# Kernel optimization log

Measured on AMD Instinct MI355X. Metric: run time of the kernel, lower is better.

## Reference

```python
import jax, jax.numpy as jnp
import numpy as np

N, E, G = 150000, 300000, 4096   # nodes, edges, graphs
H, L = 256, 7                    # hidden_channels, num_gc_layers
ATOM_FEATS, ATOM_VOCAB = 9, 64
BOND_FEATS, BOND_VOCAB = 3, 8
BN_EPS = 1e-5
MSG_EPS = 1e-7


def setup_inputs() -> dict:
    key = jax.random.key(0)
    ks = jax.random.split(key, 10)
    return dict(
        x=jax.random.randint(ks[0], (N, ATOM_FEATS), 0, ATOM_VOCAB),
        edge_index=jax.random.randint(ks[1], (2, E), 0, N),
        edge_attr=jax.random.randint(ks[2], (E, BOND_FEATS), 0, BOND_VOCAB),
        batch=jnp.sort(jax.random.randint(ks[3], (N,), 0, G)),
        atom_emb=jax.random.normal(ks[4], (ATOM_FEATS, ATOM_VOCAB, H), jnp.float32) * 0.02,
        bond_emb=jax.random.normal(ks[5], (BOND_FEATS, BOND_VOCAB, H), jnp.float32) * 0.02,
        vn_weight=jnp.zeros((1, H), jnp.float32),  # Embedding(1,H) init to 0
        conv_w=jax.random.normal(ks[6], (L, H, H), jnp.float32) / np.float32(np.sqrt(H)),
        conv_b=jnp.zeros((L, H), jnp.float32),
        norm_gamma=jnp.ones((L, H), jnp.float32),
        norm_beta=jnp.zeros((L, H), jnp.float32),
        vn_w=jax.random.normal(ks[7], (L - 1, 2, H, H), jnp.float32) / np.float32(np.sqrt(H)),
        vn_b=jnp.zeros((L - 1, 2, H), jnp.float32),
        vn_gamma=jnp.ones((L - 1, 2, H), jnp.float32),
        vn_beta=jnp.zeros((L - 1, 2, H), jnp.float32),
    )


def _bn(x, gamma, beta):
    # BatchNorm1d in training mode (biased batch stats over the node axis)
    mu = jnp.mean(x, axis=0)
    var = jnp.mean(jnp.square(x - mu), axis=0)
    return (x - mu) * jax.lax.rsqrt(var + BN_EPS) * gamma + beta


def _genconv(h, src, dst, edge_emb, w, b):
    # GENConv, aggr='add', mlp_layers=1: msg = relu(x_j + e) + eps; out = Linear(x + sum_agg)
    msg = jax.nn.relu(h[src] + edge_emb) + MSG_EPS            # [E,H]
    agg = jax.ops.segment_sum(msg, dst, num_segments=N)       # [N,H]
    return (h + agg) @ w + b


def reference(x, edge_index, edge_attr, batch, atom_emb, bond_emb, vn_weight,
              conv_w, conv_b, norm_gamma, norm_beta, vn_w, vn_b, vn_gamma, vn_beta):
    src, dst = edge_index[0], edge_index[1]
    # AtomEncoder: sum of per-feature embeddings
    h = jnp.take(atom_emb[0], x[:, 0], axis=0)
    for f in range(1, ATOM_FEATS):
        h = h + jnp.take(atom_emb[f], x[:, f], axis=0)
    # virtual node embedding (one per graph, gathered init from Embedding(1,H))
    vn = jnp.broadcast_to(vn_weight[0], (G, H))
    h = h + vn[batch]
    # BondEncoder (conv_encode_edge=False -> encode once)
    edge_emb = jnp.take(bond_emb[0], edge_attr[:, 0], axis=0)
    for f in range(1, BOND_FEATS):
        edge_emb = edge_emb + jnp.take(bond_emb[f], edge_attr[:, f], axis=0)
    # res+ block: GENConv -> [BN -> ReLU -> VN update -> GENConv -> +res]*
    h = _genconv(h, src, dst, edge_emb, conv_w[0], conv_b[0])
    for layer in range(1, L):
        h2 = jax.nn.relu(_bn(h, norm_gamma[layer - 1], norm_beta[layer - 1]))
        # virtual node: pool + residual, 2-layer MLP (Linear->BN->ReLU twice)
        vn_t = jax.ops.segment_sum(h2, batch, num_segments=G) + vn
        for j in range(2):
            vn_t = jax.nn.relu(_bn(vn_t @ vn_w[layer - 1, j] + vn_b[layer - 1, j],
                                   vn_gamma[layer - 1, j], vn_beta[layer - 1, j]))
        vn = vn_t
        h2 = h2 + vn[batch]
        h = _genconv(h2, src, dst, edge_emb, conv_w[layer], conv_b[layer]) + h
    h = _bn(h, norm_gamma[L - 1], norm_beta[L - 1])
    return jax.ops.segment_sum(h, batch, num_segments=G)  # global_add_pool -> [G,H]
```

## Files before the change

kernel.cpp:

```cpp
#include <hip/hip_runtime.h>
#include <hip/hip_bf16.h>


#define Ncnt 150000
#define Ecnt 300000
#define Gcnt 4096
#define Hc 256
#define Lcnt 7
#define BN_EPS 1e-5f
#define MSG_EPS 1e-7f

typedef __hip_bfloat16 bf16;
typedef __attribute__((ext_vector_type(8))) short bf16x8;
typedef __attribute__((ext_vector_type(8))) unsigned short u16x8;
typedef __attribute__((ext_vector_type(4))) float f32x4;

static __device__ __forceinline__ int imin(int a, int b) { return a < b ? a : b; }

static __device__ __forceinline__ float bs2f(unsigned short s) {
  unsigned u = ((unsigned)s) << 16;
  union { unsigned u; float f; } c; c.u = u; return c.f;
}
static __device__ __forceinline__ unsigned short f2bs(float f) {
  bf16 h = __float2bfloat16(f);
  union { bf16 h; unsigned short s; } c; c.h = h; return c.s;
}
static __device__ __forceinline__ float4 bf4tof4(ushort4 u) {
  float4 r; r.x = bs2f(u.x); r.y = bs2f(u.y); r.z = bs2f(u.z); r.w = bs2f(u.w); return r;
}
static __device__ __forceinline__ ushort4 f4tobf4(float4 v) {
  ushort4 u; u.x = f2bs(v.x); u.y = f2bs(v.y); u.z = f2bs(v.z); u.w = f2bs(v.w); return u;
}

static __device__ __forceinline__ void gll16(const bf16* g, const short* l) {
  __builtin_amdgcn_global_load_lds((const __attribute__((address_space(1))) void*)g,
                                   (__attribute__((address_space(3))) void*)l, 16, 0, 0);
}

__global__ __launch_bounds__(256) void k_zero(float* __restrict__ p, int n) {
  int i = blockIdx.x * 256 + threadIdx.x;
  if (i < n) p[i] = 0.f;
}
__global__ __launch_bounds__(256) void k_zero_int(int* __restrict__ p, int n) {
  int i = blockIdx.x * 256 + threadIdx.x;
  if (i < n) p[i] = 0;
}
__global__ __launch_bounds__(256) void k_copy4(float* __restrict__ dst, const float* __restrict__ src, int n4) {
  int i = blockIdx.x * 256 + threadIdx.x;
  if (i < n4) ((float4*)dst)[i] = ((const float4*)src)[i];
}
__global__ void k_diag(float* __restrict__ out, float v) { out[0] = v; }

__global__ __launch_bounds__(256) void k_count(const int* __restrict__ ei, int* __restrict__ cnt) {
  int e = blockIdx.x * 256 + threadIdx.x;
  if (e < Ecnt) atomicAdd(&cnt[ei[Ecnt + e]], 1);
}
__global__ __launch_bounds__(256) void k_scan1(const int* __restrict__ cnt, int* __restrict__ rowptr,
                                               int* __restrict__ bsum, int n) {
  __shared__ int sh[256];
  int t = threadIdx.x;
  int i = blockIdx.x * 256 + t;
  int v = (i < n) ? cnt[i] : 0;
  sh[t] = v;
  __syncthreads();
#pragma unroll
  for (int off = 1; off < 256; off <<= 1) {
    int u = (t >= off) ? sh[t - off] : 0;
    __syncthreads();
    sh[t] += u;
    __syncthreads();
  }
  if (i < n) rowptr[i] = sh[t] - v;
  if (t == 255) bsum[blockIdx.x] = sh[255];
}
__global__ __launch_bounds__(1024) void k_scan2(int* __restrict__ bsum, int nb) {
  __shared__ int sh[1024];
  int t = threadIdx.x;
  int v = (t < nb) ? bsum[t] : 0;
  sh[t] = v;
  __syncthreads();
#pragma unroll
  for (int off = 1; off < 1024; off <<= 1) {
    int u = (t >= off) ? sh[t - off] : 0;
    __syncthreads();
    sh[t] += u;
    __syncthreads();
  }
  if (t < nb) bsum[t] = sh[t] - v;
}
__global__ __launch_bounds__(256) void k_scan3(int* __restrict__ rowptr, int* __restrict__ cursor,
                                               const int* __restrict__ bsum, int n) {
  int i = blockIdx.x * 256 + threadIdx.x;
  if (i < n) {
    int v = rowptr[i] + bsum[blockIdx.x];
    rowptr[i] = v;
    cursor[i] = v;
  }
  if (i == 0) rowptr[n] = Ecnt;
}
__global__ __launch_bounds__(256) void k_scatter(const int* __restrict__ ei, int* __restrict__ cursor,
                                                 int* __restrict__ eidx) {
  int e = blockIdx.x * 256 + threadIdx.x;
  if (e < Ecnt) {
    int d = ei[Ecnt + e];
    int pos = atomicAdd(&cursor[d], 1);
    eidx[pos] = e;
  }
}

__global__ __launch_bounds__(256) void k_prep_w(const float* __restrict__ W, bf16* __restrict__ hi,
                                                bf16* __restrict__ lo, int nmats) {
  int c = blockIdx.x * 256 + threadIdx.x;
  if (c >= nmats * 8192) return;
  int lane = c & 63;
  int t = c >> 6;
  int kc8 = t & 7;
  int nt = (t >> 3) & 15;
  int m = t >> 7;
  int n = nt * 16 + (lane & 15);
  int k0 = kc8 * 32 + (lane >> 4) * 8;
  bf16x8 hv, lv;
#pragma unroll
  for (int j = 0; j < 8; ++j) {
    float w = W[(size_t)m * 65536 + (size_t)(k0 + j) * 256 + n];
    unsigned short h = f2bs(w);
    float res = w - bs2f(h);
    hv[j] = (short)h;
    lv[j] = (short)f2bs(res);
  }
  *(bf16x8*)&hi[(size_t)c * 8] = hv;
  *(bf16x8*)&lo[(size_t)c * 8] = lv;
}

__global__ __launch_bounds__(256) void k_atom_encode(const int* __restrict__ x,
                                                     const float* __restrict__ aemb,
                                                     const float* __restrict__ vnw,
                                                     bf16* __restrict__ P) {
  int wave = threadIdx.x >> 6, lane = threadIdx.x & 63;
  int r = blockIdx.x * 4 + wave;
  if (r >= Ncnt) return;
  int c4 = lane * 4;
  const int* xr = x + (size_t)r * 9;
  float4 v = *(const float4*)&vnw[c4];
#pragma unroll
  for (int f = 0; f < 9; ++f) {
    float4 e = *(const float4*)&aemb[(size_t)((f << 6) + xr[f]) * Hc + c4];
    v.x += e.x; v.y += e.y; v.z += e.z; v.w += e.w;
  }
  *(ushort4*)&P[(size_t)r * Hc + c4] = f4tobf4(v);
}

__global__ __launch_bounds__(256) void k_init_vn(float* __restrict__ vn, const float* __restrict__ vnw) {
  int idx = blockIdx.x * 256 + threadIdx.x;
  vn[idx] = vnw[idx & (Hc - 1)];
}

__global__ __launch_bounds__(256) void k_agg(const bf16* __restrict__ P, bf16* __restrict__ T,
                                             const int* __restrict__ rowptr, const int* __restrict__ eidx,
                                             const int* __restrict__ ei, const int* __restrict__ ea,
                                             const float* __restrict__ bemb,
                                             const float* __restrict__ vn, const int* __restrict__ batch,
                                             const float* __restrict__ stats,
                                             const float* __restrict__ gamma, const float* __restrict__ beta,
                                             float invM) {
  int wave = threadIdx.x >> 6, lane = threadIdx.x & 63;
  int r = blockIdx.x * 4 + wave;
  if (r >= Ncnt) return;
  int c4 = lane * 4;
  bool hasbn = (stats != nullptr);
  float4 scv = make_float4(1.f, 1.f, 1.f, 1.f), bbv = make_float4(0.f, 0.f, 0.f, 0.f);
  if (hasbn) {
    float4 sv = *(const float4*)&stats[c4];
    float4 qv = *(const float4*)&stats[Hc + c4];
    float4 gv = *(const float4*)&gamma[c4];
    float4 bv = *(const float4*)&beta[c4];
    float mu, var;
    mu = sv.x * invM; var = qv.x * invM - mu * mu; scv.x = rsqrtf(var + BN_EPS) * gv.x; bbv.x = bv.x - mu * scv.x;
    mu = sv.y * invM; var = qv.y * invM - mu * mu; scv.y = rsqrtf(var + BN_EPS) * gv.y; bbv.y = bv.y - mu * scv.y;
    mu = sv.z * invM; var = qv.z * invM - mu * mu; scv.z = rsqrtf(var + BN_EPS) * gv.z; bbv.z = bv.z - mu * scv.z;
    mu = sv.w * invM; var = qv.w * invM - mu * mu; scv.w = rsqrtf(var + BN_EPS) * gv.w; bbv.w = bv.w - mu * scv.w;
  }
  float4 acc;
  {
    float4 v = bf4tof4(*(const ushort4*)&P[(size_t)r * Hc + c4]);
    if (hasbn) {
      v.x = fmaxf(fmaf(v.x, scv.x, bbv.x), 0.f); v.y = fmaxf(fmaf(v.y, scv.y, bbv.y), 0.f);
      v.z = fmaxf(fmaf(v.z, scv.z, bbv.z), 0.f); v.w = fmaxf(fmaf(v.w, scv.w, bbv.w), 0.f);
      const float4 w = *(const float4*)&vn[(size_t)batch[r] * Hc + c4];
      v.x += w.x; v.y += w.y; v.z += w.z; v.w += w.w;
    }
    acc = v;
  }
  int j1 = rowptr[r + 1];
  for (int j = rowptr[r]; j < j1; ++j) {
    int e = eidx[j];
    int s = ei[e];
    int a0 = ea[e * 3], a1 = ea[e * 3 + 1], a2 = ea[e * 3 + 2];
    float4 em = *(const float4*)&bemb[(size_t)a0 * Hc + c4];
    float4 e1 = *(const float4*)&bemb[(size_t)(8 + a1) * Hc + c4];
    float4 e2 = *(const float4*)&bemb[(size_t)(16 + a2) * Hc + c4];
    em.x += e1.x + e2.x; em.y += e1.y + e2.y; em.z += e1.z + e2.z; em.w += e1.w + e2.w;
    float4 v = bf4tof4(*(const ushort4*)&P[(size_t)s * Hc + c4]);
    if (hasbn) {
      v.x = fmaxf(fmaf(v.x, scv.x, bbv.x), 0.f); v.y = fmaxf(fmaf(v.y, scv.y, bbv.y), 0.f);
      v.z = fmaxf(fmaf(v.z, scv.z, bbv.z), 0.f); v.w = fmaxf(fmaf(v.w, scv.w, bbv.w), 0.f);
      const float4 w = *(const float4*)&vn[(size_t)batch[s] * Hc + c4];
      v.x += w.x; v.y += w.y; v.z += w.z; v.w += w.w;
    }
    acc.x += fmaxf(v.x + em.x, 0.f) + MSG_EPS;
    acc.y += fmaxf(v.y + em.y, 0.f) + MSG_EPS;
    acc.z += fmaxf(v.z + em.z, 0.f) + MSG_EPS;
    acc.w += fmaxf(v.w + em.w, 0.f) + MSG_EPS;
  }
  *(ushort4*)&T[(size_t)r * Hc + c4] = f4tobf4(acc);
}

__global__ __launch_bounds__(256) void k_seg_vn(const bf16* __restrict__ P, const int* __restrict__ batch,
                                                float* __restrict__ vnt, const float* __restrict__ stats,
                                                const float* __restrict__ gamma, const float* __restrict__ beta,
                                                float invM) {
  int wave = threadIdx.x >> 6, lane = threadIdx.x & 63;
  int base = (blockIdx.x * 4 + wave) * 64;
  if (base >= Ncnt) return;
  int c4 = lane * 4;
  float4 sv = *(const float4*)&stats[c4];
  float4 qv = *(const float4*)&stats[Hc + c4];
  float4 gv = *(const float4*)&gamma[c4];
  float4 bv = *(const float4*)&beta[c4];
  float4 scv, bbv;
  float mu, var;
  mu = sv.x * invM; var = qv.x * invM - mu * mu; scv.x = rsqrtf(var + BN_EPS) * gv.x; bbv.x = bv.x - mu * scv.x;
  mu = sv.y * invM; var = qv.y * invM - mu * mu; scv.y = rsqrtf(var + BN_EPS) * gv.y; bbv.y = bv.y - mu * scv.y;
  mu = sv.z * invM; var = qv.z * invM - mu * mu; scv.z = rsqrtf(var + BN_EPS) * gv.z; bbv.z = bv.z - mu * scv.z;
  mu = sv.w * invM; var = qv.w * invM - mu * mu; scv.w = rsqrtf(var + BN_EPS) * gv.w; bbv.w = bv.w - mu * scv.w;
  int end = imin(base + 64, Ncnt);
  float4 acc = make_float4(0.f, 0.f, 0.f, 0.f);
  int curg = batch[base];
  for (int r = base; r < end; ++r) {
    int g = batch[r];
    float4 v = bf4tof4(*(const ushort4*)&P[(size_t)r * Hc + c4]);
    v.x = fmaxf(fmaf(v.x, scv.x, bbv.x), 0.f); v.y = fmaxf(fmaf(v.y, scv.y, bbv.y), 0.f);
    v.z = fmaxf(fmaf(v.z, scv.z, bbv.z), 0.f); v.w = fmaxf(fmaf(v.w, scv.w, bbv.w), 0.f);
    if (g != curg) {
      float* d = &vnt[(size_t)curg * Hc + c4];
      atomicAdd(d, acc.x); atomicAdd(d + 1, acc.y); atomicAdd(d + 2, acc.z); atomicAdd(d + 3, acc.w);
      acc = make_float4(0.f, 0.f, 0.f, 0.f);
      curg = g;
    }
    acc.x += v.x; acc.y += v.y; acc.z += v.z; acc.w += v.w;
  }
  float* d = &vnt[(size_t)curg * Hc + c4];
  atomicAdd(d, acc.x); atomicAdd(d + 1, acc.y); atomicAdd(d + 2, acc.z); atomicAdd(d + 3, acc.w);
}

__global__ __launch_bounds__(256) void k_vn_relu(const float* __restrict__ in, float* __restrict__ out,
                                                 const float* __restrict__ stats,
                                                 const float* __restrict__ gamma, const float* __restrict__ beta,
                                                 float invM) {
  int idx = blockIdx.x * 256 + threadIdx.x;
  int c = idx & (Hc - 1);
  float mu = stats[c] * invM;
  float var = stats[Hc + c] * invM - mu * mu;
  float sc = rsqrtf(var + BN_EPS) * gamma[c];
  float bb = beta[c] - mu * sc;
  out[idx] = fmaxf(fmaf(in[idx], sc, bb), 0.f);
}

__global__ __launch_bounds__(256) void k_bn_pool(const bf16* __restrict__ P, const int* __restrict__ batch,
                                                 float* __restrict__ out, const float* __restrict__ stats,
                                                 const float* __restrict__ gamma, const float* __restrict__ beta,
                                                 float invM) {
  int wave = threadIdx.x >> 6, lane = threadIdx.x & 63;
  int base = (blockIdx.x * 4 + wave) * 64;
  if (base >= Ncnt) return;
  int c4 = lane * 4;
  float4 sv = *(const float4*)&stats[c4];
  float4 qv = *(const float4*)&stats[Hc + c4];
  float4 gv = *(const float4*)&gamma[c4];
  float4 bv = *(const float4*)&beta[c4];
  float4 scv, bbv;
  float mu, var;
  mu = sv.x * invM; var = qv.x * invM - mu * mu; scv.x = rsqrtf(var + BN_EPS) * gv.x; bbv.x = bv.x - mu * scv.x;
  mu = sv.y * invM; var = qv.y * invM - mu * mu; scv.y = rsqrtf(var + BN_EPS) * gv.y; bbv.y = bv.y - mu * scv.y;
  mu = sv.z * invM; var = qv.z * invM - mu * mu; scv.z = rsqrtf(var + BN_EPS) * gv.z; bbv.z = bv.z - mu * scv.z;
  mu = sv.w * invM; var = qv.w * invM - mu * mu; scv.w = rsqrtf(var + BN_EPS) * gv.w; bbv.w = bv.w - mu * scv.w;
  int end = imin(base + 64, Ncnt);
  float4 acc = make_float4(0.f, 0.f, 0.f, 0.f);
  int curg = batch[base];
  for (int r = base; r < end; ++r) {
    int g = batch[r];
    float4 v = bf4tof4(*(const ushort4*)&P[(size_t)r * Hc + c4]);
    v.x = fmaf(v.x, scv.x, bbv.x); v.y = fmaf(v.y, scv.y, bbv.y);
    v.z = fmaf(v.z, scv.z, bbv.z); v.w = fmaf(v.w, scv.w, bbv.w);
    if (g != curg) {
      float* d = &out[(size_t)curg * Hc + c4];
      atomicAdd(d, acc.x); atomicAdd(d + 1, acc.y); atomicAdd(d + 2, acc.z); atomicAdd(d + 3, acc.w);
      acc = make_float4(0.f, 0.f, 0.f, 0.f);
      curg = g;
    }
    acc.x += v.x; acc.y += v.y; acc.z += v.z; acc.w += v.w;
  }
  float* d = &out[(size_t)curg * Hc + c4];
  atomicAdd(d, acc.x); atomicAdd(d + 1, acc.y); atomicAdd(d + 2, acc.z); atomicAdd(d + 3, acc.w);
}

__global__ __launch_bounds__(256, 2) void k_gemm_mfma(const bf16* __restrict__ A, const bf16* __restrict__ Whi,
                                                      const bf16* __restrict__ Wlo, const float* __restrict__ bias,
                                                      const bf16* __restrict__ R, bf16* __restrict__ C,
                                                      float* __restrict__ stats, int M) {
  __shared__ __attribute__((aligned(16))) short As[128 * 64];
  __shared__ __attribute__((aligned(16))) float Cs[32 * 258];
  __shared__ float lsum[256], lsq[256];
  int tid = threadIdx.x;
  int wave = tid >> 6, lane = tid & 63;
  int quad = lane >> 4, l15 = lane & 15;
  int wr = (wave & 1) * 64;
  int wc = (wave >> 1) * 128;
  int row0 = blockIdx.x * 128;

  lsum[tid] = 0.f;
  lsq[tid] = 0.f;

  int sr[4], sjg[4];
#pragma unroll
  for (int i = 0; i < 4; ++i) {
    int s = i * 256 + tid;
    sr[i] = s >> 3;
    sjg[i] = (s & 7) ^ (sr[i] & 7);
  }

  f32x4 acc[4][8];
#pragma unroll
  for (int i = 0; i < 4; ++i)
#pragma unroll
    for (int j = 0; j < 8; ++j) acc[i][j] = (f32x4){0.f, 0.f, 0.f, 0.f};

  for (int kci = 0; kci < 4; ++kci) {
    int kc = kci * 64;
#pragma unroll
    for (int i = 0; i < 4; ++i) {
      int ar = row0 + sr[i]; if (ar >= M) ar = M - 1;
      gll16(A + (size_t)ar * Hc + kc + sjg[i] * 8, &As[(i * 256 + wave * 64) * 8]);
    }
    __syncthreads();
#pragma unroll
    for (int ks = 0; ks < 2; ++ks) {
      int kc8 = kci * 2 + ks;
      int g = ks * 4 + quad;
      bf16x8 af[4];
#pragma unroll
      for (int mi = 0; mi < 4; ++mi) {
        int row = wr + mi * 16 + l15;
        af[mi] = *(const bf16x8*)&As[row * 64 + (g ^ (row & 7)) * 8];
      }
#pragma unroll
      for (int nii = 0; nii < 8; ++nii) {
        int nt = (wave >> 1) * 8 + nii;
        size_t fo = (((size_t)nt * 8 + kc8) * 64 + lane) * 8;
        bf16x8 bh = *(const bf16x8*)&Whi[fo];
        bf16x8 bl = *(const bf16x8*)&Wlo[fo];
#pragma unroll
        for (int mi = 0; mi < 4; ++mi) {
          acc[mi][nii] = __builtin_amdgcn_mfma_f32_16x16x32_bf16(af[mi], bh, acc[mi][nii], 0, 0, 0);
          acc[mi][nii] = __builtin_amdgcn_mfma_f32_16x16x32_bf16(af[mi], bl, acc[mi][nii], 0, 0, 0);
        }
      }
    }
    __syncthreads();
  }

  float s8[8], q8[8];
#pragma unroll
  for (int k = 0; k < 8; ++k) { s8[k] = 0.f; q8[k] = 0.f; }
  int c8 = (tid & 31) * 8;

  for (int p = 0; p < 4; ++p) {
    int lr0 = (wave & 1) * 16 + quad * 4;
#pragma unroll
    for (int ni = 0; ni < 8; ++ni) {
      int col = wc + ni * 16 + l15;
      float bcol = bias[col];
#pragma unroll
      for (int j = 0; j < 4; ++j)
        Cs[(lr0 + j) * 258 + col] = acc[p][ni][j] + bcol;
    }
    __syncthreads();
#pragma unroll
    for (int i = 0; i < 4; ++i) {
      int gsl = i * 256 + tid;
      int lr = gsl >> 5;
      int grow = row0 + ((lr < 16) ? p * 16 + lr : 48 + p * 16 + lr);
      if (grow < M) {
        const float* src = &Cs[lr * 258 + c8];
        float v[8];
#pragma unroll
        for (int k = 0; k < 8; ++k) v[k] = src[k];
        if (R) {
          u16x8 rv = *(const u16x8*)&R[(size_t)grow * Hc + c8];
#pragma unroll
          for (int k = 0; k < 8; ++k) v[k] += bs2f(rv[k]);
        }
        u16x8 ov;
#pragma unroll
        for (int k = 0; k < 8; ++k) {
          ov[k] = f2bs(v[k]);
          s8[k] += v[k];
          q8[k] = fmaf(v[k], v[k], q8[k]);
        }
        *(u16x8*)&C[(size_t)grow * Hc + c8] = ov;
      }
    }
    __syncthreads();
  }

#pragma unroll
  for (int k = 0; k < 8; ++k) {
    atomicAdd(&lsum[c8 + k], s8[k]);
    atomicAdd(&lsq[c8 + k], q8[k]);
  }
  __syncthreads();
  atomicAdd(&stats[tid], lsum[tid]);
  atomicAdd(&stats[Hc + tid], lsq[tid]);
}

__global__ __launch_bounds__(256) void k_gemm_f32(const float* __restrict__ A, const float* __restrict__ W,
                                                  const float* __restrict__ bias, float* __restrict__ C,
                                                  float* __restrict__ statsOut,
                                                  const float* __restrict__ statsIn,
                                                  const float* __restrict__ gIn, const float* __restrict__ bIn,
                                                  float invM, int M) {
  __shared__ float As[64][68];
  __shared__ float Ws[64][68];
  __shared__ float lsum[64], lsq[64];
  int tid = threadIdx.x;
  int row0 = blockIdx.x * 64;
  int col0 = blockIdx.y * 64;
  int tx = tid & 15, ty = tid >> 4;
  if (tid < 64) { lsum[tid] = 0.f; lsq[tid] = 0.f; }
  float acc[4][4] = {{0.f}};
  for (int k0 = 0; k0 < 256; k0 += 64) {
#pragma unroll
    for (int i = 0; i < 4; ++i) {
      int lin = tid + i * 256;
      int r = lin >> 4;
      int c4 = (lin & 15) << 2;
      int gr = row0 + r;
      float4 v = make_float4(0.f, 0.f, 0.f, 0.f);
      if (gr < M) v = *(const float4*)&A[(size_t)gr * Hc + k0 + c4];
      if (statsIn) {
        float4 sv = *(const float4*)&statsIn[k0 + c4];
        float4 qv = *(const float4*)&statsIn[Hc + k0 + c4];
        float4 gv = *(const float4*)&gIn[k0 + c4];
        float4 bv = *(const float4*)&bIn[k0 + c4];
        float mu, var, sc, bb;
        mu = sv.x * invM; var = qv.x * invM - mu * mu; sc = rsqrtf(var + BN_EPS) * gv.x; bb = bv.x - mu * sc;
        v.x = fmaxf(fmaf(v.x, sc, bb), 0.f);
        mu = sv.y * invM; var = qv.y * invM - mu * mu; sc = rsqrtf(var + BN_EPS) * gv.y; bb = bv.y - mu * sc;
        v.y = fmaxf(fmaf(v.y, sc, bb), 0.f);
        mu = sv.z * invM; var = qv.z * invM - mu * mu; sc = rsqrtf(var + BN_EPS) * gv.z; bb = bv.z - mu * sc;
        v.z = fmaxf(fmaf(v.z, sc, bb), 0.f);
        mu = sv.w * invM; var = qv.w * invM - mu * mu; sc = rsqrtf(var + BN_EPS) * gv.w; bb = bv.w - mu * sc;
        v.w = fmaxf(fmaf(v.w, sc, bb), 0.f);
      }
      As[r][c4] = v.x; As[r][c4 + 1] = v.y; As[r][c4 + 2] = v.z; As[r][c4 + 3] = v.w;
      float4 w = *(const float4*)&W[(size_t)(k0 + r) * Hc + col0 + c4];
      Ws[r][c4] = w.x; Ws[r][c4 + 1] = w.y; Ws[r][c4 + 2] = w.z; Ws[r][c4 + 3] = w.w;
    }
    __syncthreads();
#pragma unroll
    for (int k = 0; k < 64; ++k) {
      float a[4], w[4];
#pragma unroll
      for (int i = 0; i < 4; ++i) a[i] = As[ty * 4 + i][k];
#pragma unroll
      for (int j = 0; j < 4; ++j) w[j] = Ws[k][tx * 4 + j];
#pragma unroll
      for (int i = 0; i < 4; ++i)
#pragma unroll
        for (int j = 0; j < 4; ++j) acc[i][j] = fmaf(a[i], w[j], acc[i][j]);
    }
    __syncthreads();
  }
  float cs[4] = {0.f, 0.f, 0.f, 0.f}, cq[4] = {0.f, 0.f, 0.f, 0.f};
#pragma unroll
  for (int i = 0; i < 4; ++i) {
    int gr = row0 + ty * 4 + i;
    if (gr >= M) break;
#pragma unroll
    for (int j = 0; j < 4; ++j) {
      int gc = col0 + tx * 4 + j;
      float v = acc[i][j] + bias[gc];
      C[(size_t)gr * Hc + gc] = v;
      cs[j] += v;
      cq[j] = fmaf(v, v, cq[j]);
    }
  }
#pragma unroll
  for (int j = 0; j < 4; ++j) {
    atomicAdd(&lsum[tx * 4 + j], cs[j]);
    atomicAdd(&lsq[tx * 4 + j], cq[j]);
  }
  __syncthreads();
  if (tid < 64) {
    atomicAdd(&statsOut[col0 + tid], lsum[tid]);
    atomicAdd(&statsOut[Hc + col0 + tid], lsq[tid]);
  }
}

extern "C" void kernel_launch(void* const* d_in, const int* in_sizes, int n_in,
                              void* d_out, int out_size, void* d_ws, size_t ws_size,
                              hipStream_t stream) {
  const int* x = (const int*)d_in[0];
  const int* ei = (const int*)d_in[1];
  const int* ea = (const int*)d_in[2];
  const int* batch = (const int*)d_in[3];
  const float* aemb = (const float*)d_in[4];
  const float* bemb = (const float*)d_in[5];
  const float* vnw = (const float*)d_in[6];
  const float* conv_w = (const float*)d_in[7];
  const float* conv_b = (const float*)d_in[8];
  const float* ngamma = (const float*)d_in[9];
  const float* nbeta = (const float*)d_in[10];
  const float* vn_w = (const float*)d_in[11];
  const float* vn_b = (const float*)d_in[12];
  const float* vn_g = (const float*)d_in[13];
  const float* vn_be = (const float*)d_in[14];
  float* out = (float*)d_out;

  const size_t NODE = (size_t)Ncnt * Hc;
  const size_t GH = (size_t)Gcnt * Hc;
  const int nScanBlk = (Ncnt + 255) / 256;

  size_t off = 0;
  char* base = (char*)d_ws;
  auto take = [&](size_t bytes) { size_t o = off; off += (bytes + 15) & ~(size_t)15; return o; };
  float* vn = (float*)(base + take(GH * 4));
  float* vnt = (float*)(base + take(GH * 4));
  float* vnu = (float*)(base + take(GH * 4));
  float* vnv = (float*)(base + take(GH * 4));
  float* statsN = (float*)(base + take(2 * Hc * 4));
  float* statsV1 = (float*)(base + take(2 * Hc * 4));
  float* statsV2 = (float*)(base + take(2 * Hc * 4));
  int* rowptr = (int*)(base + take((size_t)(Ncnt + 1) * 4));
  int* cursor = (int*)(base + take((size_t)Ncnt * 4));
  int* eidx = (int*)(base + take((size_t)Ecnt * 4));
  int* bsum = (int*)(base + take((size_t)nScanBlk * 4));
  bf16* P = (bf16*)(base + take(NODE * 2));
  bf16* T = (bf16*)(base + take(NODE * 2));
  bf16* WhiC = (bf16*)(base + take((size_t)Lcnt * 65536 * 2));
  bf16* WloC = (bf16*)(base + take((size_t)Lcnt * 65536 * 2));
  const size_t NEED = off;
  if (ws_size < NEED) {
    k_zero<<<(int)((GH + 255) / 256), 256, 0, stream>>>(out, (int)GH);
    k_diag<<<1, 1, 0, stream>>>(out, 100000.f + (float)(ws_size / (1024.0 * 1024.0)));
    return;
  }

  const int eBlk = (Ecnt + 255) / 256;
  const int nWaveBlk = (Ncnt + 3) / 4;
  const int segBlk = (Ncnt + 255) / 256;
  const int ggN = (Ncnt + 127) / 128;
  const dim3 gv(Gcnt / 64, 4);
  const float invN = 1.f / Ncnt;
  const float invG = 1.f / Gcnt;

  k_zero_int<<<nScanBlk, 256, 0, stream>>>(cursor, Ncnt);
  k_count<<<eBlk, 256, 0, stream>>>(ei, cursor);
  k_scan1<<<nScanBlk, 256, 0, stream>>>(cursor, rowptr, bsum, Ncnt);
  k_scan2<<<1, 1024, 0, stream>>>(bsum, nScanBlk);
  k_scan3<<<nScanBlk, 256, 0, stream>>>(rowptr, cursor, bsum, Ncnt);
  k_scatter<<<eBlk, 256, 0, stream>>>(ei, cursor, eidx);

  k_prep_w<<<(Lcnt * 8192 + 255) / 256, 256, 0, stream>>>(conv_w, WhiC, WloC, Lcnt);

  k_atom_encode<<<nWaveBlk, 256, 0, stream>>>(x, aemb, vnw, P);
  k_init_vn<<<(int)(GH / 256), 256, 0, stream>>>(vn, vnw);
  k_agg<<<nWaveBlk, 256, 0, stream>>>(P, T, rowptr, eidx, ei, ea, bemb,
                                      nullptr, nullptr, nullptr, nullptr, nullptr, 0.f);
  k_zero<<<2, 256, 0, stream>>>(statsN, 2 * Hc);
  k_gemm_mfma<<<ggN, 256, 0, stream>>>(T, WhiC, WloC, conv_b, nullptr, P, statsN, Ncnt);

  for (int l = 1; l < Lcnt; ++l) {
    int p = l - 1;
    const float* g = ngamma + (size_t)p * Hc;
    const float* b = nbeta + (size_t)p * Hc;
    k_copy4<<<(int)(GH / 1024), 256, 0, stream>>>(vnt, vn, (int)(GH / 4));
    k_seg_vn<<<segBlk, 256, 0, stream>>>(P, batch, vnt, statsN, g, b, invN);
    k_zero<<<2, 256, 0, stream>>>(statsV1, 2 * Hc);
    k_gemm_f32<<<gv, 256, 0, stream>>>(vnt, vn_w + (size_t)(2 * p) * 65536,
                                       vn_b + (size_t)(2 * p) * Hc, vnu, statsV1,
                                       nullptr, nullptr, nullptr, invG, Gcnt);
    k_zero<<<2, 256, 0, stream>>>(statsV2, 2 * Hc);
    k_gemm_f32<<<gv, 256, 0, stream>>>(vnu, vn_w + (size_t)(2 * p + 1) * 65536,
                                       vn_b + (size_t)(2 * p + 1) * Hc, vnv, statsV2,
                                       statsV1, vn_g + (size_t)(2 * p) * Hc,
                                       vn_be + (size_t)(2 * p) * Hc, invG, Gcnt);
    k_vn_relu<<<(int)(GH / 256), 256, 0, stream>>>(vnv, vn, statsV2,
                                                   vn_g + (size_t)(2 * p + 1) * Hc,
                                                   vn_be + (size_t)(2 * p + 1) * Hc, invG);
    k_agg<<<nWaveBlk, 256, 0, stream>>>(P, T, rowptr, eidx, ei, ea, bemb, vn, batch, statsN, g, b, invN);
    k_zero<<<2, 256, 0, stream>>>(statsN, 2 * Hc);
    k_gemm_mfma<<<ggN, 256, 0, stream>>>(T, WhiC + (size_t)l * 65536, WloC + (size_t)l * 65536,
                                         conv_b + (size_t)l * Hc, P, P, statsN, Ncnt);
  }

  k_zero<<<(int)((GH + 255) / 256), 256, 0, stream>>>(out, (int)GH);
  k_bn_pool<<<segBlk, 256, 0, stream>>>(P, batch, out, statsN,
                                        ngamma + (size_t)(Lcnt - 1) * Hc, nbeta + (size_t)(Lcnt - 1) * Hc,
                                        invN);
}
```

Before: 2.534 ms.

## Pack CSR edge records with source and bond/graph ids, widen aggregation per-lane

The scatter step now writes a packed int2 record per CSR edge holding the source node plus the three bond attributes and the source's graph id. The aggregation kernel therefore no longer does indirect loads through eidx, ei, ea and batch for each edge. The aggregation kernel also moves from one 64-lane wave per node with 4 channels per lane to 32 lanes per node with 8 channels each (16-byte bf16 loads), and prefetches the next edge record. The BN scale and shift are computed once in a small kernel instead of in every thread, at the cost of one extra tiny launch per layer.

```diff
diff --git a/kernel.cpp b/kernel.cpp
--- a/kernel.cpp
+++ b/kernel.cpp
@@ -50,6 +50,17 @@
   if (i < n4) ((float4*)dst)[i] = ((const float4*)src)[i];
 }
 __global__ void k_diag(float* __restrict__ out, float v) { out[0] = v; }
+
+__global__ __launch_bounds__(256) void k_bnprep(const float* __restrict__ stats,
+                                                const float* __restrict__ gamma, const float* __restrict__ beta,
+                                                float* __restrict__ scb, float* __restrict__ bbb, float invM) {
+  int c = threadIdx.x;
+  float mu = stats[c] * invM;
+  float var = stats[Hc + c] * invM - mu * mu;
+  float sc = rsqrtf(var + BN_EPS) * gamma[c];
+  scb[c] = sc;
+  bbb[c] = beta[c] - mu * sc;
+}
 
 __global__ __launch_bounds__(256) void k_count(const int* __restrict__ ei, int* __restrict__ cnt) {
   int e = blockIdx.x * 256 + threadIdx.x;
@@ -98,13 +109,16 @@
   }
   if (i == 0) rowptr[n] = Ecnt;
 }
-__global__ __launch_bounds__(256) void k_scatter(const int* __restrict__ ei, int* __restrict__ cursor,
-                                                 int* __restrict__ eidx) {
+__global__ __launch_bounds__(256) void k_scatter(const int* __restrict__ ei, const int* __restrict__ ea,
+                                                 const int* __restrict__ batch, int* __restrict__ cursor,
+                                                 int2* __restrict__ erec) {
   int e = blockIdx.x * 256 + threadIdx.x;
   if (e < Ecnt) {
     int d = ei[Ecnt + e];
+    int s = ei[e];
+    int packed = ea[e * 3] | (ea[e * 3 + 1] << 3) | (ea[e * 3 + 2] << 6) | (batch[s] << 9);
     int pos = atomicAdd(&cursor[d], 1);
-    eidx[pos] = e;
+    erec[pos] = make_int2(s, packed);
   }
 }
 
@@ -156,83 +170,88 @@
 }
 
 __global__ __launch_bounds__(256) void k_agg(const bf16* __restrict__ P, bf16* __restrict__ T,
-                                             const int* __restrict__ rowptr, const int* __restrict__ eidx,
-                                             const int* __restrict__ ei, const int* __restrict__ ea,
+                                             const int* __restrict__ rowptr, const int2* __restrict__ erec,
                                              const float* __restrict__ bemb,
                                              const float* __restrict__ vn, const int* __restrict__ batch,
-                                             const float* __restrict__ stats,
-                                             const float* __restrict__ gamma, const float* __restrict__ beta,
-                                             float invM) {
-  int wave = threadIdx.x >> 6, lane = threadIdx.x & 63;
-  int r = blockIdx.x * 4 + wave;
+                                             const float* __restrict__ scb, const float* __restrict__ bbb) {
+  int hw = threadIdx.x >> 5, lane = threadIdx.x & 31;
+  int r = blockIdx.x * 8 + hw;
   if (r >= Ncnt) return;
-  int c4 = lane * 4;
-  bool hasbn = (stats != nullptr);
-  float4 scv = make_float4(1.f, 1.f, 1.f, 1.f), bbv = make_float4(0.f, 0.f, 0.f, 0.f);
+  int c8 = lane * 8;
+  bool hasbn = (scb != nullptr);
+  float sc[8], bb[8];
   if (hasbn) {
-    float4 sv = *(const float4*)&stats[c4];
-    float4 qv = *(const float4*)&stats[Hc + c4];
-    float4 gv = *(const float4*)&gamma[c4];
-    float4 bv = *(const float4*)&beta[c4];
-    float mu, var;
-    mu = sv.x * invM; var = qv.x * invM - mu * mu; scv.x = rsqrtf(var + BN_EPS) * gv.x; bbv.x = bv.x - mu * scv.x;
-    mu = sv.y * invM; var = qv.y * invM - mu * mu; scv.y = rsqrtf(var + BN_EPS) * gv.y; bbv.y = bv.y - mu * scv.y;
-    mu = sv.z * invM; var = qv.z * invM - mu * mu; scv.z = rsqrtf(var + BN_EPS) * gv.z; bbv.z = bv.z - mu * scv.z;
-    mu = sv.w * invM; var = qv.w * invM - mu * mu; scv.w = rsqrtf(var + BN_EPS) * gv.w; bbv.w = bv.w - mu * scv.w;
-  }
-  float4 acc;
+    float4 s0 = *(const float4*)&scb[c8], s1 = *(const float4*)&scb[c8 + 4];
+    float4 b0 = *(const float4*)&bbb[c8], b1 = *(const float4*)&bbb[c8 + 4];
+    sc[0] = s0.x; sc[1] = s0.y; sc[2] = s0.z; sc[3] = s0.w;
+    sc[4] = s1.x; sc[5] = s1.y; sc[6] = s1.z; sc[7] = s1.w;
+    bb[0] = b0.x; bb[1] = b0.y; bb[2] = b0.z; bb[3] = b0.w;
+    bb[4] = b1.x; bb[5] = b1.y; bb[6] = b1.z; bb[7] = b1.w;
+  }
+  float acc[8];
   {
-    float4 v = bf4tof4(*(const ushort4*)&P[(size_t)r * Hc + c4]);
+    u16x8 pv = *(const u16x8*)&P[(size_t)r * Hc + c8];
     if (hasbn) {
-      v.x = fmaxf(fmaf(v.x, scv.x, bbv.x), 0.f); v.y = fmaxf(fmaf(v.y, scv.y, bbv.y), 0.f);
-      v.z = fmaxf(fmaf(v.z, scv.z, bbv.z), 0.f); v.w = fmaxf(fmaf(v.w, scv.w, bbv.w), 0.f);
-      const float4 w = *(const float4*)&vn[(size_t)batch[r] * Hc + c4];
-      v.x += w.x; v.y += w.y; v.z += w.z; v.w += w.w;
-    }
-    acc = v;
-  }
-  int j1 = rowptr[r + 1];
-  for (int j = rowptr[r]; j < j1; ++j) {
-    int e = eidx[j];
-    int s = ei[e];
-    int a0 = ea[e * 3], a1 = ea[e * 3 + 1], a2 = ea[e * 3 + 2];
-    float4 em = *(const float4*)&bemb[(size_t)a0 * Hc + c4];
-    float4 e1 = *(const float4*)&bemb[(size_t)(8 + a1) * Hc + c4];
-    float4 e2 = *(const float4*)&bemb[(size_t)(16 + a2) * Hc + c4];
-    em.x += e1.x + e2.x; em.y += e1.y + e2.y; em.z += e1.z + e2.z; em.w += e1.w + e2.w;
-    float4 v = bf4tof4(*(const ushort4*)&P[(size_t)s * Hc + c4]);
-    if (hasbn) {
-      v.x = fmaxf(fmaf(v.x, scv.x, bbv.x), 0.f); v.y = fmaxf(fmaf(v.y, scv.y, bbv.y), 0.f);
-      v.z = fmaxf(fmaf(v.z, scv.z, bbv.z), 0.f); v.w = fmaxf(fmaf(v.w, scv.w, bbv.w), 0.f);
-      const float4 w = *(const float4*)&vn[(size_t)batch[s] * Hc + c4];
-      v.x += w.x; v.y += w.y; v.z += w.z; v.w += w.w;
-    }
-    acc.x += fmaxf(v.x + em.x, 0.f) + MSG_EPS;
-    acc.y += fmaxf(v.y + em.y, 0.f) + MSG_EPS;
-    acc.z += fmaxf(v.z + em.z, 0.f) + MSG_EPS;
-    acc.w += fmaxf(v.w + em.w, 0.f) + MSG_EPS;
-  }
-  *(ushort4*)&T[(size_t)r * Hc + c4] = f4tobf4(acc);
+      const float* vr = &vn[(size_t)batch[r] * Hc + c8];
+      float4 w0 = *(const float4*)vr, w1 = *(const float4*)(vr + 4);
+      float w[8] = {w0.x, w0.y, w0.z, w0.w, w1.x, w1.y, w1.z, w1.w};
+#pragma unroll
+      for (int k = 0; k < 8; ++k) acc[k] = fmaxf(fmaf(bs2f(pv[k]), sc[k], bb[k]), 0.f) + w[k];
+    } else {
+#pragma unroll
+      for (int k = 0; k < 8; ++k) acc[k] = bs2f(pv[k]);
+    }
+  }
+  int j0 = rowptr[r], j1 = rowptr[r + 1];
+  if (j0 < j1) {
+    int2 er = erec[j0];
+    for (int j = j0; j < j1; ++j) {
+      int2 ern = (j + 1 < j1) ? erec[j + 1] : er;
+      int s = er.x;
+      int a0 = er.y & 7, a1 = (er.y >> 3) & 7, a2 = (er.y >> 6) & 7, g = er.y >> 9;
+      u16x8 sv = *(const u16x8*)&P[(size_t)s * Hc + c8];
+      const float* e0 = &bemb[(size_t)a0 * Hc + c8];
+      const float* e1 = &bemb[(size_t)(8 + a1) * Hc + c8];
+      const float* e2 = &bemb[(size_t)(16 + a2) * Hc + c8];
+      float4 e0a = *(const float4*)e0, e0b = *(const float4*)(e0 + 4);
+      float4 e1a = *(const float4*)e1, e1b = *(const float4*)(e1 + 4);
+      float4 e2a = *(const float4*)e2, e2b = *(const float4*)(e2 + 4);
+      float em[8] = {e0a.x + e1a.x + e2a.x, e0a.y + e1a.y + e2a.y,
+                     e0a.z + e1a.z + e2a.z, e0a.w + e1a.w + e2a.w,
+                     e0b.x + e1b.x + e2b.x, e0b.y + e1b.y + e2b.y,
+                     e0b.z + e1b.z + e2b.z, e0b.w + e1b.w + e2b.w};
+      if (hasbn) {
+        const float* vr = &vn[(size_t)g * Hc + c8];
+        float4 w0 = *(const float4*)vr, w1 = *(const float4*)(vr + 4);
+        float w[8] = {w0.x, w0.y, w0.z, w0.w, w1.x, w1.y, w1.z, w1.w};
+#pragma unroll
+        for (int k = 0; k < 8; ++k) {
+          float v = fmaxf(fmaf(bs2f(sv[k]), sc[k], bb[k]), 0.f) + w[k];
+          acc[k] += fmaxf(v + em[k], 0.f) + MSG_EPS;
+        }
+      } else {
+#pragma unroll
+        for (int k = 0; k < 8; ++k)
+          acc[k] += fmaxf(bs2f(sv[k]) + em[k], 0.f) + MSG_EPS;
+      }
+      er = ern;
+    }
+  }
+  u16x8 ov;
+#pragma unroll
+  for (int k = 0; k < 8; ++k) ov[k] = f2bs(acc[k]);
+  *(u16x8*)&T[(size_t)r * Hc + c8] = ov;
 }
 
 __global__ __launch_bounds__(256) void k_seg_vn(const bf16* __restrict__ P, const int* __restrict__ batch,
-                                                float* __restrict__ vnt, const float* __restrict__ stats,
-                                                const float* __restrict__ gamma, const float* __restrict__ beta,
-                                                float invM) {
+                                                float* __restrict__ vnt,
+                                                const float* __restrict__ scb, const float* __restrict__ bbb) {
   int wave = threadIdx.x >> 6, lane = threadIdx.x & 63;
   int base = (blockIdx.x * 4 + wave) * 64;
   if (base >= Ncnt) return;
   int c4 = lane * 4;
-  float4 sv = *(const float4*)&stats[c4];
-  float4 qv = *(const float4*)&stats[Hc + c4];
-  float4 gv = *(const float4*)&gamma[c4];
-  float4 bv = *(const float4*)&beta[c4];
-  float4 scv, bbv;
-  float mu, var;
-  mu = sv.x * invM; var = qv.x * invM - mu * mu; scv.x = rsqrtf(var + BN_EPS) * gv.x; bbv.x = bv.x - mu * scv.x;
-  mu = sv.y * invM; var = qv.y * invM - mu * mu; scv.y = rsqrtf(var + BN_EPS) * gv.y; bbv.y = bv.y - mu * scv.y;
-  mu = sv.z * invM; var = qv.z * invM - mu * mu; scv.z = rsqrtf(var + BN_EPS) * gv.z; bbv.z = bv.z - mu * scv.z;
-  mu = sv.w * invM; var = qv.w * invM - mu * mu; scv.w = rsqrtf(var + BN_EPS) * gv.w; bbv.w = bv.w - mu * scv.w;
+  float4 scv = *(const float4*)&scb[c4];
+  float4 bbv = *(const float4*)&bbb[c4];
   int end = imin(base + 64, Ncnt);
   float4 acc = make_float4(0.f, 0.f, 0.f, 0.f);
   int curg = batch[base];
@@ -267,23 +286,14 @@
 }
 
 __global__ __launch_bounds__(256) void k_bn_pool(const bf16* __restrict__ P, const int* __restrict__ batch,
-                                                 float* __restrict__ out, const float* __restrict__ stats,
-                                                 const float* __restrict__ gamma, const float* __restrict__ beta,
-                                                 float invM) {
+                                                 float* __restrict__ out,
+                                                 const float* __restrict__ scb, const float* __restrict__ bbb) {
   int wave = threadIdx.x >> 6, lane = threadIdx.x & 63;
   int base = (blockIdx.x * 4 + wave) * 64;
   if (base >= Ncnt) return;
   int c4 = lane * 4;
-  float4 sv = *(const float4*)&stats[c4];
-  float4 qv = *(const float4*)&stats[Hc + c4];
-  float4 gv = *(const float4*)&gamma[c4];
-  float4 bv = *(const float4*)&beta[c4];
-  float4 scv, bbv;
-  float mu, var;
-  mu = sv.x * invM; var = qv.x * invM - mu * mu; scv.x = rsqrtf(var + BN_EPS) * gv.x; bbv.x = bv.x - mu * scv.x;
-  mu = sv.y * invM; var = qv.y * invM - mu * mu; scv.y = rsqrtf(var + BN_EPS) * gv.y; bbv.y = bv.y - mu * scv.y;
-  mu = sv.z * invM; var = qv.z * invM - mu * mu; scv.z = rsqrtf(var + BN_EPS) * gv.z; bbv.z = bv.z - mu * scv.z;
-  mu = sv.w * invM; var = qv.w * invM - mu * mu; scv.w = rsqrtf(var + BN_EPS) * gv.w; bbv.w = bv.w - mu * scv.w;
+  float4 scv = *(const float4*)&scb[c4];
+  float4 bbv = *(const float4*)&bbb[c4];
   int end = imin(base + 64, Ncnt);
   float4 acc = make_float4(0.f, 0.f, 0.f, 0.f);
   int curg = batch[base];
@@ -541,9 +551,11 @@
   float* statsN = (float*)(base + take(2 * Hc * 4));
   float* statsV1 = (float*)(base + take(2 * Hc * 4));
   float* statsV2 = (float*)(base + take(2 * Hc * 4));
+  float* scbN = (float*)(base + take(Hc * 4));
+  float* bbbN = (float*)(base + take(Hc * 4));
   int* rowptr = (int*)(base + take((size_t)(Ncnt + 1) * 4));
   int* cursor = (int*)(base + take((size_t)Ncnt * 4));
-  int* eidx = (int*)(base + take((size_t)Ecnt * 4));
+  int2* erec = (int2*)(base + take((size_t)Ecnt * 8));
   int* bsum = (int*)(base + take((size_t)nScanBlk * 4));
   bf16* P = (bf16*)(base + take(NODE * 2));
   bf16* T = (bf16*)(base + take(NODE * 2));
@@ -558,6 +570,7 @@
 
   const int eBlk = (Ecnt + 255) / 256;
   const int nWaveBlk = (Ncnt + 3) / 4;
+  const int aggBlk = (Ncnt + 7) / 8;
   const int segBlk = (Ncnt + 255) / 256;
   const int ggN = (Ncnt + 127) / 128;
   const dim3 gv(Gcnt / 64, 4);
@@ -569,23 +582,22 @@
   k_scan1<<<nScanBlk, 256, 0, stream>>>(cursor, rowptr, bsum, Ncnt);
   k_scan2<<<1, 1024, 0, stream>>>(bsum, nScanBlk);
   k_scan3<<<nScanBlk, 256, 0, stream>>>(rowptr, cursor, bsum, Ncnt);
-  k_scatter<<<eBlk, 256, 0, stream>>>(ei, cursor, eidx);
+  k_scatter<<<eBlk, 256, 0, stream>>>(ei, ea, batch, cursor, erec);
 
   k_prep_w<<<(Lcnt * 8192 + 255) / 256, 256, 0, stream>>>(conv_w, WhiC, WloC, Lcnt);
 
   k_atom_encode<<<nWaveBlk, 256, 0, stream>>>(x, aemb, vnw, P);
   k_init_vn<<<(int)(GH / 256), 256, 0, stream>>>(vn, vnw);
-  k_agg<<<nWaveBlk, 256, 0, stream>>>(P, T, rowptr, eidx, ei, ea, bemb,
-                                      nullptr, nullptr, nullptr, nullptr, nullptr, 0.f);
+  k_agg<<<aggBlk, 256, 0, stream>>>(P, T, rowptr, erec, bemb, nullptr, nullptr, nullptr, nullptr);
   k_zero<<<2, 256, 0, stream>>>(statsN, 2 * Hc);
   k_gemm_mfma<<<ggN, 256, 0, stream>>>(T, WhiC, WloC, conv_b, nullptr, P, statsN, Ncnt);
 
   for (int l = 1; l < Lcnt; ++l) {
     int p = l - 1;
-    const float* g = ngamma + (size_t)p * Hc;
-    const float* b = nbeta + (size_t)p * Hc;
+    k_bnprep<<<1, 256, 0, stream>>>(statsN, ngamma + (size_t)p * Hc, nbeta + (size_t)p * Hc,
+                                    scbN, bbbN, invN);
     k_copy4<<<(int)(GH / 1024), 256, 0, stream>>>(vnt, vn, (int)(GH / 4));
-    k_seg_vn<<<segBlk, 256, 0, stream>>>(P, batch, vnt, statsN, g, b, invN);
+    k_seg_vn<<<segBlk, 256, 0, stream>>>(P, batch, vnt, scbN, bbbN);
     k_zero<<<2, 256, 0, stream>>>(statsV1, 2 * Hc);
     k_gemm_f32<<<gv, 256, 0, stream>>>(vnt, vn_w + (size_t)(2 * p) * 65536,
                                        vn_b + (size_t)(2 * p) * Hc, vnu, statsV1,
@@ -598,14 +610,14 @@
     k_vn_relu<<<(int)(GH / 256), 256, 0, stream>>>(vnv, vn, statsV2,
                                                    vn_g + (size_t)(2 * p + 1) * Hc,
                                                    vn_be + (size_t)(2 * p + 1) * Hc, invG);
-    k_agg<<<nWaveBlk, 256, 0, stream>>>(P, T, rowptr, eidx, ei, ea, bemb, vn, batch, statsN, g, b, invN);
+    k_agg<<<aggBlk, 256, 0, stream>>>(P, T, rowptr, erec, bemb, vn, batch, scbN, bbbN);
     k_zero<<<2, 256, 0, stream>>>(statsN, 2 * Hc);
     k_gemm_mfma<<<ggN, 256, 0, stream>>>(T, WhiC + (size_t)l * 65536, WloC + (size_t)l * 65536,
                                          conv_b + (size_t)l * Hc, P, P, statsN, Ncnt);
   }
 
+  k_bnprep<<<1, 256, 0, stream>>>(statsN, ngamma + (size_t)(Lcnt - 1) * Hc,
+                                  nbeta + (size_t)(Lcnt - 1) * Hc, scbN, bbbN, invN);
   k_zero<<<(int)((GH + 255) / 256), 256, 0, stream>>>(out, (int)GH);
-  k_bn_pool<<<segBlk, 256, 0, stream>>>(P, batch, out, statsN,
-                                        ngamma + (size_t)(Lcnt - 1) * Hc, nbeta + (size_t)(Lcnt - 1) * Hc,
-                                        invN);
-}
+  k_bn_pool<<<segBlk, 256, 0, stream>>>(P, batch, out, scbN, bbbN);
+}
```

Measured after the change: 2.291 ms. 9.6% less time.
